# Kernel tuning notes

Hardware: AMD Instinct MI355X
Metric: run time of the kernel (lower is better)

Reference implementation:

```python
import jax, jax.numpy as jnp
import numpy as np

TOPK = 32
NUM_PT = 8192
NUM_KP = 8
HW = 19200


def _conv3(x, w, b):
    # x: [1, C, N], w: [O, C, 3] -> [1, O, N] (padding=1)
    y = jax.lax.conv_general_dilated(x, w, (1,), [(1, 1)],
                                     dimension_numbers=('NCH', 'OIH', 'NCH'))
    return y + b[None, :, None]


def setup_inputs() -> dict:
    key = jax.random.key(0)
    ks = jax.random.split(key, 64)

    def p(i, *shape):
        return (jax.random.normal(ks[i], shape, dtype=jnp.float32) * 0.05)

    inp = {
        'seg': jax.random.uniform(ks[0], (1, NUM_PT), dtype=jnp.float32),
        'img': jax.random.normal(ks[1], (1, 32, HW), dtype=jnp.float32),
        'cloud': jax.random.normal(ks[2], (1, NUM_PT, 3), dtype=jnp.float32),
        't': jax.random.normal(ks[3], (1, 3), dtype=jnp.float32),
        'choose': jax.random.randint(ks[4], (1, 1, NUM_PT), 0, HW),
        # Pseudo3DConv params (all 1x1 conv1d == channel matmul)
        'pconv1_w': p(5, 64, 3),    'pconv1_b': p(6, 64),
        'pconv2_w': p(7, 128, 64),  'pconv2_b': p(8, 128),
        'conv1_w': p(9, 64, 32),    'conv1_b': p(10, 64),
        'conv2_w': p(11, 128, 64),  'conv2_b': p(12, 128),
        'psconv1_w': p(13, 256, 128), 'psconv1_b': p(14, 256),
        'psconv2_w': p(15, 128, 256), 'psconv2_b': p(16, 128),
        'final_w': p(17, 128, 416), 'final_b': p(18, 128),
        # heads
        'seg1_w': p(19, 64, 128, 3), 'seg1_b': p(20, 64),
        'seg2_w': p(21, 32, 64),     'seg2_b': p(22, 32),
        'seg3_w': p(23, 1, 32),      'seg3_b': p(24, 1),
        'dis1_w': p(25, 64, 128, 3), 'dis1_b': p(26, 64),
        'dis2_w': p(27, 32, 64),     'dis2_b': p(28, 32),
        'dis3_w': p(29, 1, 32),      'dis3_b': p(30, 1),
        'lin1_w': p(31, 90, 128),    'lin1_b': p(32, 90),
        'lin2_w': p(33, 64, 90),     'lin2_b': p(34, 64),
        'lin3_w': p(35, 3 * NUM_KP, 64), 'lin3_b': p(36, 3 * NUM_KP),
    }
    return inp


def reference(seg, img, cloud, t, choose,
              pconv1_w, pconv1_b, pconv2_w, pconv2_b,
              conv1_w, conv1_b, conv2_w, conv2_b,
              psconv1_w, psconv1_b, psconv2_w, psconv2_b,
              final_w, final_b,
              seg1_w, seg1_b, seg2_w, seg2_b, seg3_w, seg3_b,
              dis1_w, dis1_b, dis2_w, dis2_b, dis3_w, dis3_b,
              lin1_w, lin1_b, lin2_w, lin2_b, lin3_w, lin3_b):
    lrelu = jax.nn.leaky_relu  # slope 0.01, same as torch default
    N = NUM_PT

    # gather per-point image features at chosen pixels: [N, 32]
    feat = jnp.take(img[0], choose[0, 0], axis=1).T
    c = cloud[0]  # [N, 3]

    # ---- KNN (self included, as in knn_cuda) ----
    d2 = jnp.sum((c[:, None, :] - c[None, :, :]) ** 2, axis=-1)  # [N, N]
    _, idx = jax.lax.top_k(-d2, TOPK)  # [N, K] nearest neighbors

    # ---- point-feature MLP (pconv1 -> lrelu -> pconv2) ----
    pf = lrelu(c @ pconv1_w.T + pconv1_b) @ pconv2_w.T + pconv2_b  # [N, 128]

    # ---- vectorized per-point neighbor gather + MLP + weighted maxpool ----
    nf = feat[idx]    # [N, K, 32]
    npf = pf[idx]     # [N, K, 128]
    npos = c[idx]     # [N, K, 3]
    w = jax.nn.softmax(-jnp.linalg.norm(c[:, None, :] - npos, axis=-1), axis=1)  # [N, K]

    f = lrelu(nf @ conv1_w.T + conv1_b) @ conv2_w.T + conv2_b          # [N, K, 128]
    fp = lrelu(npf @ psconv1_w.T + psconv1_b) @ psconv2_w.T + psconv2_b  # [N, K, 128]
    f = jnp.max(f * w[..., None], axis=1)    # [N, 128]
    fp = jnp.max(fp * w[..., None], axis=1)  # [N, 128]

    # final2 = [fp | img_feat], final1 = [f | cloud_feat] -> cat -> [N, 416]
    final = jnp.concatenate([fp, feat, f, pf], axis=1)
    fused = lrelu(final) @ final_w.T + final_b  # [N, 128]
    fused = fused.T[None]  # [1, 128, N]

    def pw(x, w_, b_):  # 1x1 conv1d on [1, C, N]
        return jnp.einsum('oc,bcn->bon', w_, x) + b_[None, :, None]

    # segmentation head
    h = lrelu(_conv3(fused, seg1_w, seg1_b))
    seg_pre = pw(lrelu(pw(h, seg2_w, seg2_b)), seg3_w, seg3_b).reshape(1, N)

    # distance-to-center weighting (norm along coord dim, softmax over points)
    dis_center = jax.nn.softmax(
        jnp.linalg.norm(cloud - (-t)[:, None, :], axis=2), axis=1)  # [1, N]

    # distance head (on unweighted fused features, matching torch op order)
    h = lrelu(_conv3(fused, dis1_w, dis1_b))
    dis_pre = pw(lrelu(pw(h, dis2_w, dis2_b)), dis3_w, dis3_b).reshape(1, N)

    # weight fused features by center distance and segmentation, sum-pool
    fused = fused * dis_center[:, None, :] * seg[:, None, :]
    g = jnp.sum(fused, axis=2)  # [1, 128]

    kp = lrelu(g @ lin1_w.T + lin1_b)
    kp = lrelu(kp @ lin2_w.T + lin2_b)
    keypoints = (kp @ lin3_w.T + lin3_b).reshape(1, NUM_KP, 3)
    return keypoints, dis_pre, dis_center, seg_pre
```

## Files before the change

kernel.cpp:

```cpp
#include <hip/hip_runtime.h>
#include <math.h>

#define NPT 8192
#define HWIMG 19200
#define KCAP 128

using short8 = __attribute__((ext_vector_type(8))) short;
using f32x4  = __attribute__((ext_vector_type(4))) float;

__device__ __forceinline__ float lrelu(float x) { return x > 0.f ? x : 0.01f * x; }
__device__ __forceinline__ unsigned short f2bf(float v) {
  unsigned u = __float_as_uint(v);
  return (unsigned short)((u + 0x7fffu + ((u >> 16) & 1u)) >> 16);
}
__device__ __forceinline__ float bf2f(unsigned short h) {
  return __uint_as_float(((unsigned)h) << 16);
}
__device__ __forceinline__ void split2(float v, unsigned short& h, unsigned short& l) {
  h = f2bf(v);
  l = f2bf(v - bf2f(h));
}
__device__ __forceinline__ void mfma3(f32x4& acc, short8 ah, short8 al, short8 wh, short8 wl) {
  acc = __builtin_amdgcn_mfma_f32_16x16x32_bf16(ah, wh, acc, 0, 0, 0);
  acc = __builtin_amdgcn_mfma_f32_16x16x32_bf16(al, wh, acc, 0, 0, 0);
  acc = __builtin_amdgcn_mfma_f32_16x16x32_bf16(ah, wl, acc, 0, 0, 0);
}

__device__ __forceinline__ int swz(int o, int k, int Kc) {
  return ((((o >> 4) * Kc + (k >> 5)) << 6) + (((k >> 3) & 3) << 4) + (o & 15)) * 8 + (k & 7);
}

#define OFF_PCONV2  0
#define OFF_CONV1   8192
#define OFF_CONV2   10240
#define OFF_PSCONV1 18432
#define OFF_PSCONV2 51200
#define OFF_FINAL   83968
#define OFF_W3      137216
#define OFF_W2P     186368

#define S_C4    NPT
#define S_G     129
#define S_BIASC 128
#define S_B2C   64
#define S_FEAT  (NPT*32)
#define S_W3    49152
#define S_W2P   8192
#define S_WSPL  OFF_W3
#define PREP_TOTAL (S_C4 + S_G + S_BIASC + S_B2C + S_FEAT + S_W3 + S_W2P + S_WSPL)
__global__ void k_prep(const float* __restrict__ cloud, const int* __restrict__ choose,
                       const float* __restrict__ img,
                       const float* __restrict__ seg1_w, const float* __restrict__ dis1_w,
                       const float* __restrict__ seg1_b, const float* __restrict__ dis1_b,
                       const float* __restrict__ seg2_w, const float* __restrict__ dis2_w,
                       const float* __restrict__ seg2_b, const float* __restrict__ dis2_b,
                       const float* __restrict__ pconv2_w, const float* __restrict__ conv1_w,
                       const float* __restrict__ conv2_w, const float* __restrict__ psconv1_w,
                       const float* __restrict__ psconv2_w, const float* __restrict__ final_w,
                       float* __restrict__ c4, float* __restrict__ g,
                       float* __restrict__ biasc, float* __restrict__ bias2c,
// ... 73 lines not shown

__device__ __forceinline__ unsigned bsort32u(unsigned key, int lane) {
#pragma unroll
  for (int k = 2; k <= 64; k <<= 1) {
#pragma unroll
    for (int j = k >> 1; j > 0; j >>= 1) {
      unsigned o = __shfl_xor(key, j, 64);
      bool keepmin = (((lane & j) == 0) == ((lane & k) == 0));
      key = ((o < key) == keepmin) ? o : key;
    }
  }
  return key;
}
__device__ __forceinline__ unsigned long long bsort64(unsigned long long key, int lane) {
#pragma unroll
  for (int k = 2; k <= 64; k <<= 1) {
#pragma unroll
    for (int j = k >> 1; j > 0; j >>= 1) {
      unsigned long long o = __shfl_xor(key, j, 64);
      bool keepmin = (((lane & j) == 0) == ((lane & k) == 0));
      bool omin = o < key;
      key = (omin == keepmin) ? o : key;
    }
  }
  return key;
}
__device__ __forceinline__ unsigned long long bmerge64(unsigned long long key, int lane) {
#pragma unroll
  for (int j = 32; j > 0; j >>= 1) {
    unsigned long long o = __shfl_xor(key, j, 64);
    bool keepmin = ((lane & j) == 0);
    bool omin = o < key;
    key = (omin == keepmin) ? o : key;
  }
  return key;
}

#define MEGA_GRID 3073
__global__ __launch_bounds__(256) void k_mega(const float4* __restrict__ c4,
                                              int* __restrict__ idxo, float* __restrict__ wo,
                                              const float* __restrict__ cloud,
                                              const float* __restrict__ tvec,
                                              float* __restrict__ dc,
                                              const float* __restrict__ pconv1_w, const float* __restrict__ pconv1_b,
                                              const float* __restrict__ pconv2_b, const float* __restrict__ psconv1_b,
                                              const float* __restrict__ psconv2_b,
                                              const unsigned short* __restrict__ feat_h,
                                              const unsigned short* __restrict__ feat_l,
                                              const float* __restrict__ conv1_b, const float* __restrict__ conv2_b,
                                              const unsigned short* __restrict__ Wh,
                                              const unsigned short* __restrict__ Wl,
                                              float* __restrict__ pf, float* __restrict__ Yfp,
                                              float* __restrict__ Yf) {
  __shared__ __align__(16) char smem[24704];
  int tid = threadIdx.x, lane = tid & 63, w = tid >> 6;
  int mr = lane & 15, q = lane >> 4;
  if (blockIdx.x > 2048) {
    unsigned short* sh_h = (unsigned short*)smem;
    unsigned short* sh_l = (unsigned short*)(smem + 12288);
    int cb = blockIdx.x - 2049;
    if (cb < 512) {
      int m0 = cb * 16;
      float4 cp = c4[m0 + mr];
      short8 ah0, al0, ah1, al1;
#pragma unroll
      for (int j = 0; j < 8; ++j) {
        int c0 = q*8 + j, c1 = 32 + q*8 + j;
        float v0 = lrelu(fmaf(cp.x, pconv1_w[c0*3+0], fmaf(cp.y, pconv1_w[c0*3+1],
                          fmaf(cp.z, pconv1_w[c0*3+2], pconv1_b[c0]))));
        float v1 = lrelu(fmaf(cp.x, pconv1_w[c1*3+0], fmaf(cp.y, pconv1_w[c1*3+1],
                          fmaf(cp.z, pconv1_w[c1*3+2], pconv1_b[c1]))));
        unsigned short hh, ll;
        split2(v0, hh, ll); ah0[j] = (short)hh; al0[j] = (short)ll;
        split2(v1, hh, ll); ah1[j] = (short)hh; al1[j] = (short)ll;
      }
      f32x4 acc[2];
#pragma unroll
      for (int t = 0; t < 2; ++t) { f32x4 z = {0.f,0.f,0.f,0.f}; acc[t] = z; }
      const unsigned short* W2h = Wh + OFF_PCONV2;
      const unsigned short* W2l = Wl + OFF_PCONV2;
#pragma unroll
      for (int tt = 0; tt < 2; ++tt) {
        int t1 = 2*w + tt;
        int w0 = ((t1*2 + 0)*64 + lane)*8, w1 = ((t1*2 + 1)*64 + lane)*8;
        mfma3(acc[tt], ah0, al0, *(const short8*)(W2h + w0), *(const short8*)(W2l + w0));
        mfma3(acc[tt], ah1, al1, *(const short8*)(W2h + w1), *(const short8*)(W2l + w1));
      }
#pragma unroll
      for (int tt = 0; tt < 2; ++tt) {
        int t1 = 2*w + tt, n = t1*16 + mr;
        float b = pconv2_b[n];
        int ks2 = t1 >> 1, q2 = (t1 & 1)*2 + (mr >> 3), jd = mr & 7;
#pragma unroll
        for (int r = 0; r < 4; ++r) {
          int row = q*4 + r;
          float v = acc[tt][r] + b;
          pf[(size_t)(m0+row)*128 + n] = v;
          unsigned short hh, ll; split2(v, hh, ll);
          int p = ((ks2*16 + row)*4 + q2)*8 + jd;
          sh_h[p] = hh; sh_l[p] = ll;
        }
      }
      __syncthreads();
      f32x4 acc2[4];
#pragma unroll
      for (int t = 0; t < 4; ++t) { f32x4 z = {0.f,0.f,0.f,0.f}; acc2[t] = z; }
      const unsigned short* W3h = Wh + OFF_PSCONV1;
      const unsigned short* W3l = Wl + OFF_PSCONV1;
#pragma unroll
      for (int ks = 0; ks < 4; ++ks) {
        int ap = ((ks*16 + mr)*4 + q)*8;
        short8 ah = *(const short8*)&sh_h[ap];
        short8 al = *(const short8*)&sh_l[ap];
#pragma unroll
        for (int tt = 0; tt < 4; ++tt) {
          int wb = (((4*w+tt)*4 + ks)*64 + lane)*8;
          mfma3(acc2[tt], ah, al, *(const short8*)(W3h + wb), *(const short8*)(W3l + wb));
        }
      }
      __syncthreads();
#pragma unroll
      for (int tt = 0; tt < 4; ++tt) {
        int t2 = 4*w + tt, n = t2*16 + mr;
        float b = psconv1_b[n];
        int ks3 = t2 >> 1, q3 = (t2 & 1)*2 + (mr >> 3), jd = mr & 7;
#pragma unroll
        for (int r = 0; r < 4; ++r) {
          int row = q*4 + r;
          float v = lrelu(acc2[tt][r] + b);
          unsigned short hh, ll; split2(v, hh, ll);
          int p = 6144 + ((ks3*16 + row)*4 + q3)*8 + jd;
          sh_h[p] = hh; sh_l[p] = ll;
        }
      }
      __syncthreads();
      f32x4 acc3[2];
#pragma unroll
      for (int t = 0; t < 2; ++t) { f32x4 z = {0.f,0.f,0.f,0.f}; acc3[t] = z; }
      const unsigned short* W4h = Wh + OFF_PSCONV2;
      const unsigned short* W4l = Wl + OFF_PSCONV2;
#pragma unroll
      for (int ks = 0; ks < 8; ++ks) {
        int ap = 6144 + ((ks*16 + mr)*4 + q)*8;
        short8 ah = *(const short8*)&sh_h[ap];
        short8 al = *(const short8*)&sh_l[ap];
#pragma unroll
        for (int tt = 0; tt < 2; ++tt) {
          int wb = (((2*w+tt)*8 + ks)*64 + lane)*8;
          mfma3(acc3[tt], ah, al, *(const short8*)(W4h + wb), *(const short8*)(W4l + wb));
        }
      }
#pragma unroll
      for (int tt = 0; tt < 2; ++tt) {
        int n = (2*w+tt)*16 + mr;
        float b = psconv2_b[n];
#pragma unroll
        for (int r = 0; r < 4; ++r)
          Yfp[(size_t)(m0 + q*4 + r)*128 + n] = acc3[tt][r] + b;
      }
    } else {
      int m0 = (cb - 512) * 16;
      int ab = ((m0 >> 4)*64 + lane)*8;
      short8 ah = *(const short8*)(feat_h + ab);
      short8 al = *(const short8*)(feat_l + ab);
      f32x4 acc = {0.f,0.f,0.f,0.f};
      const unsigned short* W1h = Wh + OFF_CONV1;
      const unsigned short* W1l = Wl + OFF_CONV1;
      {
        int wb = (w*64 + lane)*8;
        mfma3(acc, ah, al, *(const short8*)(W1h + wb), *(const short8*)(W1l + wb));
      }
      {
        int n = w*16 + mr;
        float b = conv1_b[n];
        int ks2 = n >> 5, q2 = (n >> 3) & 3, jd = mr & 7;
#pragma unroll
        for (int r = 0; r < 4; ++r) {
          int row = q*4 + r;
          float v = lrelu(acc[r] + b);
          unsigned short hh, ll; split2(v, hh, ll);
          int p = ((ks2*16 + row)*4 + q2)*8 + jd;
          sh_h[p] = hh; sh_l[p] = ll;
        }
      }
      __syncthreads();
      f32x4 acc2[2];
#pragma unroll
      for (int t = 0; t < 2; ++t) { f32x4 z = {0.f,0.f,0.f,0.f}; acc2[t] = z; }
      const unsigned short* W2h = Wh + OFF_CONV2;
      const unsigned short* W2l = Wl + OFF_CONV2;
#pragma unroll
      for (int ks = 0; ks < 2; ++ks) {
        int ap = ((ks*16 + mr)*4 + q)*8;
        short8 a2 = *(const short8*)&sh_h[ap];
        short8 a2l = *(const short8*)&sh_l[ap];
#pragma unroll
        for (int tt = 0; tt < 2; ++tt) {
          int wb = (((2*w+tt)*2 + ks)*64 + lane)*8;
          mfma3(acc2[tt], a2, a2l, *(const short8*)(W2h + wb), *(const short8*)(W2l + wb));
        }
      }
#pragma unroll
      for (int tt = 0; tt < 2; ++tt) {
// ... 63 lines not shown
    float4 vv = *(const float4*)&smin[w][lane*4];
    float m4 = fmaxf(fminf(fminf(vv.x, vv.y), fminf(vv.z, vv.w)), 0.f);
    unsigned key = bsort32u(__float_as_uint(m4), lane);
    float T = __uint_as_float(__shfl(key, 31, 64));
    if (lane == 0) sTv[w] = T * (1.f + 2e-5f) + 4e-5f;
  }
  __syncthreads();
  float T0 = sTv[0], T1 = sTv[1], T2 = sTv[2], T3 = sTv[3];
  for (int t = 0; t < 32; ++t) {
    int j = t*256 + tid;
    float4 cj = c4[j];
    float d;
#define APPEND(Q, P) { \
    float dx_ = (P).x-cj.x, dy_ = (P).y-cj.y, dz_ = (P).z-cj.z; \
    float de_ = dx_*dx_ + dy_*dy_ + dz_*dz_; \
    int p_ = atomicAdd(&scnt[Q],1); if (p_ < KCAP) { sd[Q][p_] = de_; sj[Q][p_] = j; } }
    d = DDOT(p0x,p0y,p0z,p0.w,cj); if (d <= T0) APPEND(0, p0);
    d = DDOT(p1x,p1y,p1z,p1.w,cj); if (d <= T1) APPEND(1, p1);
    d = DDOT(p2x,p2y,p2z,p2.w,cj); if (d <= T2) APPEND(2, p2);
    d = DDOT(p3x,p3y,p3z,p3.w,cj); if (d <= T3) APPEND(3, p3);
  }
  __syncthreads();
  int M = scnt[w]; if (M > KCAP) M = KCAP;
  unsigned long long key = (lane < M)
      ? (((unsigned long long)__float_as_uint(sd[w][lane]) << 32) | (unsigned)sj[w][lane])
      : ~0ull;
  key = bsort64(key, lane);
  for (int base = 64; base < M; base += 64) {
    unsigned long long nk = (base + lane < M)
        ? (((unsigned long long)__float_as_uint(sd[w][base+lane]) << 32) | (unsigned)sj[w][base+lane])
        : ~0ull;
    nk = bsort64(nk, lane);
    nk = __shfl_xor(nk, 63, 64);
    key = key < nk ? key : nk;
    key = bmerge64(key, lane);
  }
  float dsel = __uint_as_float((unsigned)(key >> 32));
  int   jsel = (int)(unsigned)(key & 0xffffffffu);
  float v = -sqrtf(dsel);
  float mx = v;
#pragma unroll
  for (int o = 1; o < 32; o <<= 1) mx = fmaxf(mx, __shfl_xor(mx, o, 64));
  float e = expf(v - mx);
  float s = e;
#pragma unroll
  for (int o = 1; o < 32; o <<= 1) s += __shfl_xor(s, o, 64);
  if (lane < 32) {
    int qd = q0 + w;
    wo[qd*32 + lane] = e / s;
    idxo[qd*32 + lane] = jsel;
  }
}

__global__ __launch_bounds__(256) void k_pool(const float* __restrict__ Yf,
                                              const float* __restrict__ Yfp,
                                              const float* __restrict__ feat,
                                              const float* __restrict__ pf,
                                              const int* __restrict__ idx,
                                              const float* __restrict__ w,
                                              unsigned short* __restrict__ finh,
                                              unsigned short* __restrict__ finl) {
  int n = blockIdx.x;
  int tid = threadIdx.x;
  __shared__ int sj[32];
  __shared__ float sw[32];
  __shared__ float part[2][4][128];
  __shared__ float sfin[416];
  if (tid < 32) { sj[tid] = idx[n*32+tid]; sw[tid] = w[n*32+tid]; }
  __syncthreads();
  int arr = tid >> 7, kq = (tid >> 5) & 3, cg = tid & 31;
  const float* Y = arr ? Yf : Yfp;
  float4 acc = {-INFINITY, -INFINITY, -INFINITY, -INFINITY};
#pragma unroll
  for (int kk = 0; kk < 8; ++kk) {
    int k = kq*8 + kk;
    float4 v = *(const float4*)&Y[(size_t)sj[k]*128 + cg*4];
    float wk = sw[k];
    acc.x = fmaxf(acc.x, wk*v.x); acc.y = fmaxf(acc.y, wk*v.y);
    acc.z = fmaxf(acc.z, wk*v.z); acc.w = fmaxf(acc.w, wk*v.w);
  }
  *(float4*)&part[arr][kq][cg*4] = acc;
  __syncthreads();
  if (tid < 64) {
    int a2 = tid >> 5, c2 = tid & 31;
    float4 m0v = *(const float4*)&part[a2][0][c2*4];
    float4 m1v = *(const float4*)&part[a2][1][c2*4];
    float4 m2v = *(const float4*)&part[a2][2][c2*4];
    float4 m3v = *(const float4*)&part[a2][3][c2*4];
    int base = a2 ? 160 : 0;
    sfin[base + c2*4 + 0] = lrelu(fmaxf(fmaxf(m0v.x, m1v.x), fmaxf(m2v.x, m3v.x)));
    sfin[base + c2*4 + 1] = lrelu(fmaxf(fmaxf(m0v.y, m1v.y), fmaxf(m2v.y, m3v.y)));
    sfin[base + c2*4 + 2] = lrelu(fmaxf(fmaxf(m0v.z, m1v.z), fmaxf(m2v.z, m3v.z)));
    sfin[base + c2*4 + 3] = lrelu(fmaxf(fmaxf(m0v.w, m1v.w), fmaxf(m2v.w, m3v.w)));
  } else if (tid < 192) {
    int c = tid - 64;
    sfin[288 + c] = lrelu(pf[n*128 + c]);
  } else if (tid < 224) {
    int c = tid - 192;
    sfin[128 + c] = lrelu(feat[n*32 + c]);
  }
  __syncthreads();
  if (tid < 104) {
    int plane = tid >= 52;
    int ck = plane ? tid - 52 : tid;
    int ks = ck >> 2, qq = ck & 3;
    int c0 = ks*32 + qq*8;
    short8 o8;
#pragma unroll
    for (int j = 0; j < 8; ++j) {
      unsigned short hh, ll; split2(sfin[c0 + j], hh, ll);
      o8[j] = (short)(plane ? ll : hh);
    }
    size_t pos = (((size_t)(n >> 4)*13 + ks)*64 + qq*16 + (n & 15))*8;
    *(short8*)((plane ? finl : finh) + pos) = o8;
  }
}

__global__ __launch_bounds__(256) void k_final(const unsigned short* __restrict__ Ah,
                                              const unsigned short* __restrict__ Al,
                                              const unsigned short* __restrict__ Wh,
                                              const unsigned short* __restrict__ Wl,
                                              const float* __restrict__ bias,
                                              unsigned short* __restrict__ Ch,
                                              unsigned short* __restrict__ Cl) {
  __shared__ float sC[16][132];
  int tid = threadIdx.x, lane = tid & 63, w = tid >> 6;
  int mr = lane & 15, q = lane >> 4;
  int mt = blockIdx.x;
  f32x4 acc[2];
#pragma unroll
  for (int t = 0; t < 2; ++t) { f32x4 z = {0.f,0.f,0.f,0.f}; acc[t] = z; }
#pragma unroll
  for (int ks = 0; ks < 13; ++ks) {
    int ab = ((mt*13 + ks)*64 + lane)*8;
    short8 ah = *(const short8*)(Ah + ab);
    short8 al = *(const short8*)(Al + ab);
#pragma unroll
    for (int tt = 0; tt < 2; ++tt) {
      int wb = (((2*w+tt)*13 + ks)*64 + lane)*8;
      mfma3(acc[tt], ah, al, *(const short8*)(Wh + wb), *(const short8*)(Wl + wb));
    }
  }
#pragma unroll
  for (int tt = 0; tt < 2; ++tt) {
    int n = (2*w+tt)*16 + mr;
    float b = bias[n];
#pragma unroll
    for (int r = 0; r < 4; ++r) sC[q*4 + r][n] = acc[tt][r] + b;
  }
  __syncthreads();
  {
    int ks = tid >> 6, q2 = (tid >> 4) & 3, mr2 = tid & 15;
    int c0 = ks*32 + q2*8;
    short8 oh, ol;
#pragma unroll
    for (int j = 0; j < 8; ++j) {
      unsigned short hh, ll; split2(sC[mr2][c0 + j], hh, ll);
      oh[j] = (short)hh; ol[j] = (short)ll;
    }
    size_t pos = ((size_t)mt*256 + tid)*8;
    *(short8*)(Ch + pos) = oh;
    *(short8*)(Cl + pos) = ol;
  }
}

__global__ __launch_bounds__(256) void k_c3head(const unsigned short* __restrict__ Ah,
                                               const unsigned short* __restrict__ Al,
                                               const unsigned short* __restrict__ Wh,
                                               const unsigned short* __restrict__ Wl,
                                               const float* __restrict__ biasc,
                                               const float* __restrict__ bias2c,
                                               const float* __restrict__ segw, const float* __restrict__ segb,
                                               const float* __restrict__ disw, const float* __restrict__ disb,
                                               float* __restrict__ osegp, float* __restrict__ odisp,
                                               const float* __restrict__ dc,
                                               const float* __restrict__ seg,
                                               float* __restrict__ g,
                                               const float* __restrict__ l1w, const float* __restrict__ l1b,
                                               const float* __restrict__ l2w, const float* __restrict__ l2b,
                                               const float* __restrict__ l3w, const float* __restrict__ l3b,
                                               float* __restrict__ o_kp) {
  int tid = threadIdx.x, lane = tid & 63, w = tid >> 6;
  int mr = lane & 15, q = lane >> 4;
  if (blockIdx.x >= 512) {
    __shared__ float sred[2048];
    __shared__ int slast;
    int b = blockIdx.x - 512;
    float pg[8] = {0.f,0.f,0.f,0.f,0.f,0.f,0.f,0.f};
    int mrr = tid & 15;
    for (int mi = 0; mi < 16; ++mi) {
      int m = b*16 + mi;
      int row = m*16 + mrr;
      float wrow = dc[row] * seg[row];
      size_t pos = ((size_t)m*256 + tid)*8;
      short8 hv = *(const short8*)(Ah + pos);
      short8 lv = *(const short8*)(Al + pos);
#pragma unroll
      for (int j = 0; j < 8; ++j)
        pg[j] += (bf2f((unsigned short)hv[j]) + bf2f((unsigned short)lv[j])) * wrow;
    }
#pragma unroll
    for (int j = 0; j < 8; ++j) sred[tid*8 + j] = pg[j];
    __syncthreads();
    if (tid < 128) {
      int ks = tid >> 5, q2 = (tid >> 3) & 3, j = tid & 7;
      float s = 0.f;
#pragma unroll
      for (int mr2 = 0; mr2 < 16; ++mr2) s += sred[((ks<<6) + (q2<<4) + mr2)*8 + j];
      atomicAdd(&g[tid], s);
    }
    __threadfence();
    __syncthreads();
    if (tid == 0) slast = (atomicAdd((int*)(g + 128), 1) == 31);
    __syncthreads();
    if (!slast) return;
    __shared__ float sg[128], s1[90], s2[64];
    if (tid < 128) sg[tid] = atomicAdd(&g[tid], 0.f);
    __syncthreads();
    if (tid < 90) {
      float a = l1b[tid];
      for (int i = 0; i < 128; ++i) a += sg[i]*l1w[tid*128+i];
      s1[tid] = lrelu(a);
    }
    __syncthreads();
    if (tid < 64) {
      float a = l2b[tid];
      for (int i = 0; i < 90; ++i) a += s1[i]*l2w[tid*90+i];
      s2[tid] = lrelu(a);
    }
    __syncthreads();
    if (tid < 24) {
      float a = l3b[tid];
      for (int i = 0; i < 64; ++i) a += s2[i]*l3w[tid*64+i];
      o_kp[tid] = a;
    }
    return;
  }
  __shared__ unsigned short t1h[2048], t1l[2048];
  __shared__ float shead[4][16][17];
  int m0 = blockIdx.x * 16;
  f32x4 acc[2];
#pragma unroll
  for (int t = 0; t < 2; ++t) { f32x4 z = {0.f,0.f,0.f,0.f}; acc[t] = z; }
  const unsigned short* W3h = Wh + OFF_W3;
  const unsigned short* W3l = Wl + OFF_W3;
#pragma unroll
  for (int ks = 0; ks < 12; ++ks) {
    int tap = ks >> 2, ksA = ks & 3;
    int ar = m0 + mr + tap - 1;
    short8 ah = {0,0,0,0,0,0,0,0}, al = {0,0,0,0,0,0,0,0};
    if (ar >= 0 && ar < NPT) {
      int ab = ((((ar >> 4)*4) + ksA)*64 + q*16 + (ar & 15))*8;
      ah = *(const short8*)(Ah + ab);
      al = *(const short8*)(Al + ab);
    }
#pragma unroll
    for (int tt = 0; tt < 2; ++tt) {
      int wb = (((2*w+tt)*12 + ks)*64 + lane)*8;
      mfma3(acc[tt], ah, al, *(const short8*)(W3h + wb), *(const short8*)(W3l + wb));
    }
  }
#pragma unroll
  for (int tt = 0; tt < 2; ++tt) {
    int t2 = 2*w + tt, n = t2*16 + mr;
    float b = biasc[n];
    int ks2 = t2 >> 1, q2 = (t2 & 1)*2 + (mr >> 3), jd = mr & 7;
#pragma unroll
    for (int r = 0; r < 4; ++r) {
      int row = q*4 + r;
      float v = lrelu(acc[tt][r] + b);
      unsigned short hh, ll; split2(v, hh, ll);
      int p = ((ks2*16 + row)*4 + q2)*8 + jd;
      t1h[p] = hh; t1l[p] = ll;
    }
  }
  __syncthreads();
  f32x4 acc2 = {0.f,0.f,0.f,0.f};
  const unsigned short* WPh = Wh + OFF_W2P;
  const unsigned short* WPl = Wl + OFF_W2P;
#pragma unroll
  for (int ks = 0; ks < 4; ++ks) {
    int ap = ((ks*16 + mr)*4 + q)*8;
    short8 ah = *(const short8*)&t1h[ap];
    short8 al = *(const short8*)&t1l[ap];
    int wb = ((w*4 + ks)*64 + lane)*8;
    mfma3(acc2, ah, al, *(const short8*)(WPh + wb), *(const short8*)(WPl + wb));
  }
  float hw = (w < 2) ? segw[w*16 + mr] : disw[(w-2)*16 + mr];
  float bb = bias2c[w*16 + mr];
#pragma unroll
  for (int r = 0; r < 4; ++r)
    shead[w][q*4 + r][mr] = lrelu(acc2[r] + bb) * hw;
  __syncthreads();
  if (tid < 16) {
    float a = 0.f;
#pragma unroll
    for (int i = 0; i < 16; ++i) a += shead[0][tid][i] + shead[1][tid][i];
    osegp[m0 + tid] = a + segb[0];
  } else if (tid < 32) {
    float a = 0.f;
#pragma unroll
    for (int i = 0; i < 16; ++i) a += shead[2][tid-16][i] + shead[3][tid-16][i];
    odisp[m0 + tid - 16] = a + disb[0];
  }
}

extern "C" void kernel_launch(void* const* d_in, const int* in_sizes, int n_in,
                              void* d_out, int out_size, void* d_ws, size_t ws_size,
                              hipStream_t stream) {
  const float* seg      = (const float*)d_in[0];
  const float* img      = (const float*)d_in[1];
  const float* cloud    = (const float*)d_in[2];
  const float* tvec     = (const float*)d_in[3];
  const int*   choose   = (const int*)d_in[4];
  const float* pconv1_w = (const float*)d_in[5];
  const float* pconv1_b = (const float*)d_in[6];
  const float* pconv2_w = (const float*)d_in[7];
  const float* pconv2_b = (const float*)d_in[8];
  const float* conv1_w  = (const float*)d_in[9];
  const float* conv1_b  = (const float*)d_in[10];
  const float* conv2_w  = (const float*)d_in[11];
  const float* conv2_b  = (const float*)d_in[12];
  const float* psconv1_w= (const float*)d_in[13];
  const float* psconv1_b= (const float*)d_in[14];
  const float* psconv2_w= (const float*)d_in[15];
  const float* psconv2_b= (const float*)d_in[16];
  const float* final_w  = (const float*)d_in[17];
  const float* final_b  = (const float*)d_in[18];
  const float* seg1_w   = (const float*)d_in[19];
  const float* seg1_b   = (const float*)d_in[20];
  const float* seg2_w   = (const float*)d_in[21];
  const float* seg2_b   = (const float*)d_in[22];
  const float* seg3_w   = (const float*)d_in[23];
  const float* seg3_b   = (const float*)d_in[24];
  const float* dis1_w   = (const float*)d_in[25];
  const float* dis1_b   = (const float*)d_in[26];
  const float* dis2_w   = (const float*)d_in[27];
  const float* dis2_b   = (const float*)d_in[28];
  const float* dis3_w   = (const float*)d_in[29];
  const float* dis3_b   = (const float*)d_in[30];
  const float* lin1_w   = (const float*)d_in[31];
  const float* lin1_b   = (const float*)d_in[32];
  const float* lin2_w   = (const float*)d_in[33];
  const float* lin2_b   = (const float*)d_in[34];
  const float* lin3_w   = (const float*)d_in[35];
  const float* lin3_b   = (const float*)d_in[36];

  float* out = (float*)d_out;
  float* ws  = (float*)d_ws;

  float* c4     = ws + 0;
  float* feat   = ws + 32768;
  unsigned short* feat_h = (unsigned short*)(ws + 294912);
  unsigned short* feat_l = (unsigned short*)(ws + 425984);
  float* pf     = ws + 557056;
  float* Yf     = ws + 1605632;
  float* Yfp    = ws + 2654208;
  int*   idx    = (int*)(ws + 3702784);
  float* wsm    = ws + 3964928;
  unsigned short* finh  = (unsigned short*)(ws + 4227072);
  unsigned short* finl  = (unsigned short*)(ws + 5931008);
  unsigned short* fusedh = (unsigned short*)(ws + 8683520);
  unsigned short* fusedl = (unsigned short*)(ws + 9207808);
  unsigned short* Wh    = (unsigned short*)(ws + 9732096);
  unsigned short* Wl    = (unsigned short*)(ws + 9829376);
  float* biasc  = ws + 9926656;
  float* bias2c = ws + 9926784;
  float* g      = ws + 9926848;

  float* o_kp   = out;
  float* o_disp = out + 24;
  float* o_dc   = out + 8216;
  float* o_segp = out + 16408;

  k_prep<<<(PREP_TOTAL + 255)/256, 256, 0, stream>>>(
      cloud, choose, img, seg1_w, dis1_w, seg1_b, dis1_b,
      seg2_w, dis2_w, seg2_b, dis2_b,
      pconv2_w, conv1_w, conv2_w, psconv1_w, psconv2_w, final_w,
      c4, g, biasc, bias2c, feat, feat_h, feat_l, Wh, Wl);

  k_mega<<<MEGA_GRID, 256, 0, stream>>>(
      (const float4*)c4, idx, wsm, cloud, tvec, o_dc,
      pconv1_w, pconv1_b, pconv2_b, psconv1_b, psconv2_b,
      feat_h, feat_l, conv1_b, conv2_b, Wh, Wl, pf, Yfp, Yf);

  k_pool<<<NPT, 256, 0, stream>>>(Yf, Yfp, feat, pf, idx, wsm, finh, finl);

  k_final<<<512, 256, 0, stream>>>(finh, finl, Wh + OFF_FINAL, Wl + OFF_FINAL,
                                   final_b, fusedh, fusedl);

  k_c3head<<<544, 256, 0, stream>>>(fusedh, fusedl, Wh, Wl, biasc, bias2c,
                                    seg3_w, seg3_b, dis3_w, dis3_b, o_segp, o_disp,
                                    o_dc, seg, g,
                                    lin1_w, lin1_b, lin2_w, lin2_b, lin3_w, lin3_b, o_kp);

  (void)in_sizes; (void)n_in; (void)out_size; (void)ws_size;
}
```

Before: 238.5 us.

## Fuse pooling, final projection and conv3 heads into one tiled tail kernel

Replaces the separate pool, final-projection and conv3-head kernels with one kernel per 16-point tile. It recomputes the max-pool and final projection for a one-point halo on each side so the 3-tap conv can read neighbours from shared memory, and it drops the finh/finl round trip through global memory. The global-feature reduction moves into its own small kernel. Separately, the psconv1→psconv2 chain in the mega kernel is split into two halves to shrink shared memory, which may raise occupancy. The cost is redundant halo work (18 rows per 16), fewer blocks in the tail (512 instead of 8192 pool blocks), and an extra sync per half.

```diff
diff --git a/kernel.cpp b/kernel.cpp
--- a/kernel.cpp
+++ b/kernel.cpp
@@ -6,6 +6,7 @@
 #define KCAP 128
 
 using short8 = __attribute__((ext_vector_type(8))) short;
+using short4v = __attribute__((ext_vector_type(4))) short;
 using f32x4  = __attribute__((ext_vector_type(4))) float;
 
 __device__ __forceinline__ float lrelu(float x) { return x > 0.f ? x : 0.01f * x; }
@@ -185,12 +186,12 @@
                                               const unsigned short* __restrict__ Wl,
                                               float* __restrict__ pf, float* __restrict__ Yfp,
                                               float* __restrict__ Yf) {
-  __shared__ __align__(16) char smem[24704];
+  __shared__ __align__(16) char smem[16384];
   int tid = threadIdx.x, lane = tid & 63, w = tid >> 6;
   int mr = lane & 15, q = lane >> 4;
   if (blockIdx.x > 2048) {
     unsigned short* sh_h = (unsigned short*)smem;
-    unsigned short* sh_l = (unsigned short*)(smem + 12288);
+    unsigned short* sh_l = (unsigned short*)(smem + 8192);
     int cb = blockIdx.x - 2049;
     if (cb < 512) {
       int m0 = cb * 16;
@@ -235,53 +236,58 @@
         }
       }
       __syncthreads();
-      f32x4 acc2[4];
-#pragma unroll
-      for (int t = 0; t < 4; ++t) { f32x4 z = {0.f,0.f,0.f,0.f}; acc2[t] = z; }
+      f32x4 acc3[2];
+#pragma unroll
+      for (int t = 0; t < 2; ++t) { f32x4 z = {0.f,0.f,0.f,0.f}; acc3[t] = z; }
       const unsigned short* W3h = Wh + OFF_PSCONV1;
       const unsigned short* W3l = Wl + OFF_PSCONV1;
-#pragma unroll
-      for (int ks = 0; ks < 4; ++ks) {
-        int ap = ((ks*16 + mr)*4 + q)*8;
-        short8 ah = *(const short8*)&sh_h[ap];
-        short8 al = *(const short8*)&sh_l[ap];
-#pragma unroll
-        for (int tt = 0; tt < 4; ++tt) {
-          int wb = (((4*w+tt)*4 + ks)*64 + lane)*8;
-          mfma3(acc2[tt], ah, al, *(const short8*)(W3h + wb), *(const short8*)(W3l + wb));
-        }
-      }
-      __syncthreads();
-#pragma unroll
-      for (int tt = 0; tt < 4; ++tt) {
-        int t2 = 4*w + tt, n = t2*16 + mr;
-        float b = psconv1_b[n];
-        int ks3 = t2 >> 1, q3 = (t2 & 1)*2 + (mr >> 3), jd = mr & 7;
-#pragma unroll
-        for (int r = 0; r < 4; ++r) {
-          int row = q*4 + r;
-          float v = lrelu(acc2[tt][r] + b);
-          unsigned short hh, ll; split2(v, hh, ll);
-          int p = 6144 + ((ks3*16 + row)*4 + q3)*8 + jd;
-          sh_h[p] = hh; sh_l[p] = ll;
-        }
-      }
-      __syncthreads();
-      f32x4 acc3[2];
-#pragma unroll
-      for (int t = 0; t < 2; ++t) { f32x4 z = {0.f,0.f,0.f,0.f}; acc3[t] = z; }
       const unsigned short* W4h = Wh + OFF_PSCONV2;
       const unsigned short* W4l = Wl + OFF_PSCONV2;
 #pragma unroll
-      for (int ks = 0; ks < 8; ++ks) {
-        int ap = 6144 + ((ks*16 + mr)*4 + q)*8;
-        short8 ah = *(const short8*)&sh_h[ap];
-        short8 al = *(const short8*)&sh_l[ap];
+      for (int h = 0; h < 2; ++h) {
+        f32x4 acc2[2];
+#pragma unroll
+        for (int t = 0; t < 2; ++t) { f32x4 z = {0.f,0.f,0.f,0.f}; acc2[t] = z; }
+#pragma unroll
+        for (int ks = 0; ks < 4; ++ks) {
+          int ap = ((ks*16 + mr)*4 + q)*8;
+          short8 ah = *(const short8*)&sh_h[ap];
+          short8 al = *(const short8*)&sh_l[ap];
+#pragma unroll
+          for (int tt = 0; tt < 2; ++tt) {
+            int ts = h*8 + 2*w + tt;
+            int wb = ((ts*4 + ks)*64 + lane)*8;
+            mfma3(acc2[tt], ah, al, *(const short8*)(W3h + wb), *(const short8*)(W3l + wb));
+          }
+        }
 #pragma unroll
         for (int tt = 0; tt < 2; ++tt) {
-          int wb = (((2*w+tt)*8 + ks)*64 + lane)*8;
-          mfma3(acc3[tt], ah, al, *(const short8*)(W4h + wb), *(const short8*)(W4l + wb));
+          int tl = 2*w + tt;
+          int n = h*128 + tl*16 + mr;
+          float b = psconv1_b[n];
+          int ks3 = tl >> 1, q3 = (tl & 1)*2 + (mr >> 3), jd = mr & 7;
+#pragma unroll
+          for (int r = 0; r < 4; ++r) {
+            int row = q*4 + r;
+            float v = lrelu(acc2[tt][r] + b);
+            unsigned short hh, ll; split2(v, hh, ll);
+            int p = 2048 + ((ks3*16 + row)*4 + q3)*8 + jd;
+            sh_h[p] = hh; sh_l[p] = ll;
+          }
         }
+        __syncthreads();
+#pragma unroll
+        for (int ks = 0; ks < 4; ++ks) {
+          int ap = 2048 + ((ks*16 + mr)*4 + q)*8;
+          short8 ah = *(const short8*)&sh_h[ap];
+          short8 al = *(const short8*)&sh_l[ap];
+#pragma unroll
+          for (int tt = 0; tt < 2; ++tt) {
+            int wb = (((2*w+tt)*8 + h*4 + ks)*64 + lane)*8;
+            mfma3(acc3[tt], ah, al, *(const short8*)(W4h + wb), *(const short8*)(W4l + wb));
+          }
+        }
+        __syncthreads();
       }
 #pragma unroll
       for (int tt = 0; tt < 2; ++tt) {
@@ -451,212 +457,153 @@
   }
 }
 
-__global__ __launch_bounds__(256) void k_pool(const float* __restrict__ Yf,
+__global__ __launch_bounds__(256) void k_tail(const float* __restrict__ Yf,
                                               const float* __restrict__ Yfp,
                                               const float* __restrict__ feat,
                                               const float* __restrict__ pf,
                                               const int* __restrict__ idx,
-                                              const float* __restrict__ w,
-                                              unsigned short* __restrict__ finh,
-                                              unsigned short* __restrict__ finl) {
-  int n = blockIdx.x;
-  int tid = threadIdx.x;
-  __shared__ int sj[32];
-  __shared__ float sw[32];
-  __shared__ float part[2][4][128];
-  __shared__ float sfin[416];
-  if (tid < 32) { sj[tid] = idx[n*32+tid]; sw[tid] = w[n*32+tid]; }
-  __syncthreads();
-  int arr = tid >> 7, kq = (tid >> 5) & 3, cg = tid & 31;
-  const float* Y = arr ? Yf : Yfp;
-  float4 acc = {-INFINITY, -INFINITY, -INFINITY, -INFINITY};
-#pragma unroll
-  for (int kk = 0; kk < 8; ++kk) {
-    int k = kq*8 + kk;
-    float4 v = *(const float4*)&Y[(size_t)sj[k]*128 + cg*4];
-    float wk = sw[k];
-    acc.x = fmaxf(acc.x, wk*v.x); acc.y = fmaxf(acc.y, wk*v.y);
-    acc.z = fmaxf(acc.z, wk*v.z); acc.w = fmaxf(acc.w, wk*v.w);
-  }
-  *(float4*)&part[arr][kq][cg*4] = acc;
-  __syncthreads();
-  if (tid < 64) {
-    int a2 = tid >> 5, c2 = tid & 31;
-    float4 m0v = *(const float4*)&part[a2][0][c2*4];
-    float4 m1v = *(const float4*)&part[a2][1][c2*4];
-    float4 m2v = *(const float4*)&part[a2][2][c2*4];
-    float4 m3v = *(const float4*)&part[a2][3][c2*4];
-    int base = a2 ? 160 : 0;
-    sfin[base + c2*4 + 0] = lrelu(fmaxf(fmaxf(m0v.x, m1v.x), fmaxf(m2v.x, m3v.x)));
-    sfin[base + c2*4 + 1] = lrelu(fmaxf(fmaxf(m0v.y, m1v.y), fmaxf(m2v.y, m3v.y)));
-    sfin[base + c2*4 + 2] = lrelu(fmaxf(fmaxf(m0v.z, m1v.z), fmaxf(m2v.z, m3v.z)));
-    sfin[base + c2*4 + 3] = lrelu(fmaxf(fmaxf(m0v.w, m1v.w), fmaxf(m2v.w, m3v.w)));
-  } else if (tid < 192) {
-    int c = tid - 64;
-    sfin[288 + c] = lrelu(pf[n*128 + c]);
-  } else if (tid < 224) {
-    int c = tid - 192;
-    sfin[128 + c] = lrelu(feat[n*32 + c]);
-  }
-  __syncthreads();
-  if (tid < 104) {
-    int plane = tid >= 52;
-    int ck = plane ? tid - 52 : tid;
-    int ks = ck >> 2, qq = ck & 3;
-    int c0 = ks*32 + qq*8;
-    short8 o8;
-#pragma unroll
-    for (int j = 0; j < 8; ++j) {
-      unsigned short hh, ll; split2(sfin[c0 + j], hh, ll);
-      o8[j] = (short)(plane ? ll : hh);
-    }
-    size_t pos = (((size_t)(n >> 4)*13 + ks)*64 + qq*16 + (n & 15))*8;
-    *(short8*)((plane ? finl : finh) + pos) = o8;
-  }
-}
-
-__global__ __launch_bounds__(256) void k_final(const unsigned short* __restrict__ Ah,
-                                              const unsigned short* __restrict__ Al,
+                                              const float* __restrict__ wsm,
                                               const unsigned short* __restrict__ Wh,
                                               const unsigned short* __restrict__ Wl,
-                                              const float* __restrict__ bias,
-                                              unsigned short* __restrict__ Ch,
-                                              unsigned short* __restrict__ Cl) {
-  __shared__ float sC[16][132];
+                                              const float* __restrict__ final_b,
+                                              const float* __restrict__ biasc,
+                                              const float* __restrict__ bias2c,
+                                              const float* __restrict__ segw, const float* __restrict__ segb,
+                                              const float* __restrict__ disw, const float* __restrict__ disb,
+                                              unsigned short* __restrict__ fusedh,
+                                              unsigned short* __restrict__ fusedl,
+                                              float* __restrict__ osegp, float* __restrict__ odisp) {
+  __shared__ int sjn[18][32];
+  __shared__ float swn[18][32];
+  __shared__ __align__(16) char sbuf[37440];
   int tid = threadIdx.x, lane = tid & 63, w = tid >> 6;
   int mr = lane & 15, q = lane >> 4;
-  int mt = blockIdx.x;
-  f32x4 acc[2];
-#pragma unroll
-  for (int t = 0; t < 2; ++t) { f32x4 z = {0.f,0.f,0.f,0.f}; acc[t] = z; }
+  int mt = blockIdx.x, m0 = mt * 16;
+  for (int t = tid; t < 18*32; t += 256) {
+    int lr = t >> 5, k = t & 31, gr = m0 - 1 + lr;
+    if (gr >= 0 && gr < NPT) { sjn[lr][k] = idx[gr*32+k]; swn[lr][k] = wsm[gr*32+k]; }
+    else { sjn[lr][k] = 0; swn[lr][k] = 0.f; }
+  }
+  __syncthreads();
+  for (int t = tid; t < 1872; t += 256) {
+    int lr, col;
+    float4 v4;
+    if (t < 1152) {
+      lr = t >> 6; int arr = (t >> 5) & 1, cg = t & 31;
+      const float* Y = arr ? Yf : Yfp;
+      float ax = -INFINITY, ay = -INFINITY, az = -INFINITY, aw = -INFINITY;
+#pragma unroll 8
+      for (int k = 0; k < 32; ++k) {
+        float4 vv = *(const float4*)&Y[(size_t)sjn[lr][k]*128 + cg*4];
+        float wk = swn[lr][k];
+        ax = fmaxf(ax, wk*vv.x); ay = fmaxf(ay, wk*vv.y);
+        az = fmaxf(az, wk*vv.z); aw = fmaxf(aw, wk*vv.w);
+      }
+      v4.x = lrelu(ax); v4.y = lrelu(ay); v4.z = lrelu(az); v4.w = lrelu(aw);
+      col = (arr ? 160 : 0) + cg*4;
+    } else if (t < 1728) {
+      int u = t - 1152; lr = u >> 5; int cg = u & 31;
+      int gr = m0 - 1 + lr;
+      int gc = gr < 0 ? 0 : (gr >= NPT ? NPT-1 : gr);
+      float4 p4 = *(const float4*)&pf[(size_t)gc*128 + cg*4];
+      v4.x = lrelu(p4.x); v4.y = lrelu(p4.y); v4.z = lrelu(p4.z); v4.w = lrelu(p4.w);
+      col = 288 + cg*4;
+    } else {
+      int u = t - 1728; lr = u >> 3; int cg = u & 7;
+      int gr = m0 - 1 + lr;
+      int gc = gr < 0 ? 0 : (gr >= NPT ? NPT-1 : gr);
+      float4 p4 = *(const float4*)&feat[(size_t)gc*32 + cg*4];
+      v4.x = lrelu(p4.x); v4.y = lrelu(p4.y); v4.z = lrelu(p4.z); v4.w = lrelu(p4.w);
+      col = 128 + cg*4;
+    }
+    int gr = m0 - 1 + lr;
+    if (gr < 0 || gr >= NPT) { v4.x = 0.f; v4.y = 0.f; v4.z = 0.f; v4.w = 0.f; }
+    int ks = col >> 5, qq = (col >> 3) & 3, j0 = col & 7;
+    char* base = sbuf + (ks*18 + lr)*80 + qq*16 + j0*2;
+    short4v hv, lv;
+    unsigned short hh, ll;
+    split2(v4.x, hh, ll); hv[0] = (short)hh; lv[0] = (short)ll;
+    split2(v4.y, hh, ll); hv[1] = (short)hh; lv[1] = (short)ll;
+    split2(v4.z, hh, ll); hv[2] = (short)hh; lv[2] = (short)ll;
+    split2(v4.w, hh, ll); hv[3] = (short)hh; lv[3] = (short)ll;
+    *(short4v*)base = hv;
+    *(short4v*)(base + 18720) = lv;
+  }
+  __syncthreads();
+  f32x4 accA[2], accB[2];
+#pragma unroll
+  for (int t = 0; t < 2; ++t) {
+    f32x4 z = {0.f,0.f,0.f,0.f}; accA[t] = z; accB[t] = z;
+  }
+  const unsigned short* WFh = Wh + OFF_FINAL;
+  const unsigned short* WFl = Wl + OFF_FINAL;
 #pragma unroll
   for (int ks = 0; ks < 13; ++ks) {
-    int ab = ((mt*13 + ks)*64 + lane)*8;
-    short8 ah = *(const short8*)(Ah + ab);
-    short8 al = *(const short8*)(Al + ab);
+    int arB = 16 + mr; if (arB > 17) arB = 17;
+    const char* pA = sbuf + (ks*18 + mr)*80 + q*16;
+    const char* pB = sbuf + (ks*18 + arB)*80 + q*16;
+    short8 ahA = *(const short8*)pA;
+    short8 alA = *(const short8*)(pA + 18720);
+    short8 ahB = *(const short8*)pB;
+    short8 alB = *(const short8*)(pB + 18720);
 #pragma unroll
     for (int tt = 0; tt < 2; ++tt) {
       int wb = (((2*w+tt)*13 + ks)*64 + lane)*8;
-      mfma3(acc[tt], ah, al, *(const short8*)(Wh + wb), *(const short8*)(Wl + wb));
-    }
-  }
-#pragma unroll
-  for (int tt = 0; tt < 2; ++tt) {
-    int n = (2*w+tt)*16 + mr;
-    float b = bias[n];
-#pragma unroll
-    for (int r = 0; r < 4; ++r) sC[q*4 + r][n] = acc[tt][r] + b;
+      short8 wh = *(const short8*)(WFh + wb);
+      short8 wl = *(const short8*)(WFl + wb);
+      mfma3(accA[tt], ahA, alA, wh, wl);
+      mfma3(accB[tt], ahB, alB, wh, wl);
+    }
+  }
+  __syncthreads();
+#pragma unroll
+  for (int tile = 0; tile < 2; ++tile) {
+#pragma unroll
+    for (int tt = 0; tt < 2; ++tt) {
+      int t2 = 2*w + tt, n = t2*16 + mr;
+      float b = final_b[n];
+      int ksA = t2 >> 1, qq = (t2 & 1)*2 + (mr >> 3), jd = mr & 7;
+#pragma unroll
+      for (int r = 0; r < 4; ++r) {
+        int lr = tile*16 + q*4 + r;
+        if (lr > 17) continue;
+        int gr = m0 - 1 + lr;
+        float v = (tile ? accB[tt][r] : accA[tt][r]) + b;
+        if (gr < 0 || gr >= NPT) v = 0.f;
+        unsigned short hh, ll; split2(v, hh, ll);
+        char* p = sbuf + (ksA*18 + lr)*80 + qq*16 + jd*2;
+        *(unsigned short*)p = hh;
+        *(unsigned short*)(p + 5760) = ll;
+      }
+    }
   }
   __syncthreads();
   {
-    int ks = tid >> 6, q2 = (tid >> 4) & 3, mr2 = tid & 15;
-    int c0 = ks*32 + q2*8;
-    short8 oh, ol;
-#pragma unroll
-    for (int j = 0; j < 8; ++j) {
-      unsigned short hh, ll; split2(sC[mr2][c0 + j], hh, ll);
-      oh[j] = (short)hh; ol[j] = (short)ll;
-    }
+    int ks2 = tid >> 6, q2 = (tid >> 4) & 3, mr2 = tid & 15;
+    int lr = mr2 + 1;
+    const char* p = sbuf + (ks2*18 + lr)*80 + q2*16;
+    short8 oh = *(const short8*)p;
+    short8 ol = *(const short8*)(p + 5760);
     size_t pos = ((size_t)mt*256 + tid)*8;
-    *(short8*)(Ch + pos) = oh;
-    *(short8*)(Cl + pos) = ol;
-  }
-}
-
-__global__ __launch_bounds__(256) void k_c3head(const unsigned short* __restrict__ Ah,
-                                               const unsigned short* __restrict__ Al,
-                                               const unsigned short* __restrict__ Wh,
-                                               const unsigned short* __restrict__ Wl,
-                                               const float* __restrict__ biasc,
-                                               const float* __restrict__ bias2c,
-                                               const float* __restrict__ segw, const float* __restrict__ segb,
-                                               const float* __restrict__ disw, const float* __restrict__ disb,
-                                               float* __restrict__ osegp, float* __restrict__ odisp,
-                                               const float* __restrict__ dc,
-                                               const float* __restrict__ seg,
-                                               float* __restrict__ g,
-                                               const float* __restrict__ l1w, const float* __restrict__ l1b,
-                                               const float* __restrict__ l2w, const float* __restrict__ l2b,
-                                               const float* __restrict__ l3w, const float* __restrict__ l3b,
-                                               float* __restrict__ o_kp) {
-  int tid = threadIdx.x, lane = tid & 63, w = tid >> 6;
-  int mr = lane & 15, q = lane >> 4;
-  if (blockIdx.x >= 512) {
-    __shared__ float sred[2048];
-    __shared__ int slast;
-    int b = blockIdx.x - 512;
-    float pg[8] = {0.f,0.f,0.f,0.f,0.f,0.f,0.f,0.f};
-    int mrr = tid & 15;
-    for (int mi = 0; mi < 16; ++mi) {
-      int m = b*16 + mi;
-      int row = m*16 + mrr;
-      float wrow = dc[row] * seg[row];
-      size_t pos = ((size_t)m*256 + tid)*8;
-      short8 hv = *(const short8*)(Ah + pos);
-      short8 lv = *(const short8*)(Al + pos);
-#pragma unroll
-      for (int j = 0; j < 8; ++j)
-        pg[j] += (bf2f((unsigned short)hv[j]) + bf2f((unsigned short)lv[j])) * wrow;
-    }
-#pragma unroll
-    for (int j = 0; j < 8; ++j) sred[tid*8 + j] = pg[j];
-    __syncthreads();
-    if (tid < 128) {
-      int ks = tid >> 5, q2 = (tid >> 3) & 3, j = tid & 7;
-      float s = 0.f;
-#pragma unroll
-      for (int mr2 = 0; mr2 < 16; ++mr2) s += sred[((ks<<6) + (q2<<4) + mr2)*8 + j];
-      atomicAdd(&g[tid], s);
-    }
-    __threadfence();
-    __syncthreads();
-    if (tid == 0) slast = (atomicAdd((int*)(g + 128), 1) == 31);
-    __syncthreads();
-    if (!slast) return;
-    __shared__ float sg[128], s1[90], s2[64];
-    if (tid < 128) sg[tid] = atomicAdd(&g[tid], 0.f);
-    __syncthreads();
-    if (tid < 90) {
-      float a = l1b[tid];
-      for (int i = 0; i < 128; ++i) a += sg[i]*l1w[tid*128+i];
-      s1[tid] = lrelu(a);
-    }
-    __syncthreads();
-    if (tid < 64) {
-      float a = l2b[tid];
-      for (int i = 0; i < 90; ++i) a += s1[i]*l2w[tid*90+i];
-      s2[tid] = lrelu(a);
-    }
-    __syncthreads();
-    if (tid < 24) {
-      float a = l3b[tid];
-      for (int i = 0; i < 64; ++i) a += s2[i]*l3w[tid*64+i];
-      o_kp[tid] = a;
-    }
-    return;
-  }
-  __shared__ unsigned short t1h[2048], t1l[2048];
-  __shared__ float shead[4][16][17];
-  int m0 = blockIdx.x * 16;
-  f32x4 acc[2];
-#pragma unroll
-  for (int t = 0; t < 2; ++t) { f32x4 z = {0.f,0.f,0.f,0.f}; acc[t] = z; }
+    *(short8*)(fusedh + pos) = oh;
+    *(short8*)(fusedl + pos) = ol;
+  }
+  f32x4 acc3[2];
+#pragma unroll
+  for (int t = 0; t < 2; ++t) { f32x4 z = {0.f,0.f,0.f,0.f}; acc3[t] = z; }
   const unsigned short* W3h = Wh + OFF_W3;
   const unsigned short* W3l = Wl + OFF_W3;
 #pragma unroll
   for (int ks = 0; ks < 12; ++ks) {
     int tap = ks >> 2, ksA = ks & 3;
-    int ar = m0 + mr + tap - 1;
-    short8 ah = {0,0,0,0,0,0,0,0}, al = {0,0,0,0,0,0,0,0};
-    if (ar >= 0 && ar < NPT) {
-      int ab = ((((ar >> 4)*4) + ksA)*64 + q*16 + (ar & 15))*8;
-      ah = *(const short8*)(Ah + ab);
-      al = *(const short8*)(Al + ab);
-    }
+    int ar = mr + tap;
+    const char* p = sbuf + (ksA*18 + ar)*80 + q*16;
+    short8 ah = *(const short8*)p;
+    short8 al = *(const short8*)(p + 5760);
 #pragma unroll
     for (int tt = 0; tt < 2; ++tt) {
       int wb = (((2*w+tt)*12 + ks)*64 + lane)*8;
-      mfma3(acc[tt], ah, al, *(const short8*)(W3h + wb), *(const short8*)(W3l + wb));
+      mfma3(acc3[tt], ah, al, *(const short8*)(W3h + wb), *(const short8*)(W3l + wb));
     }
   }
 #pragma unroll
@@ -667,40 +614,106 @@
 #pragma unroll
     for (int r = 0; r < 4; ++r) {
       int row = q*4 + r;
-      float v = lrelu(acc[tt][r] + b);
+      float v = lrelu(acc3[tt][r] + b);
       unsigned short hh, ll; split2(v, hh, ll);
-      int p = ((ks2*16 + row)*4 + q2)*8 + jd;
-      t1h[p] = hh; t1l[p] = ll;
-    }
-  }
-  __syncthreads();
-  f32x4 acc2 = {0.f,0.f,0.f,0.f};
+      char* p = sbuf + 11520 + (ks2*16 + row)*80 + q2*16 + jd*2;
+      *(unsigned short*)p = hh;
+      *(unsigned short*)(p + 5120) = ll;
+    }
+  }
+  __syncthreads();
+  f32x4 acc4 = {0.f,0.f,0.f,0.f};
   const unsigned short* WPh = Wh + OFF_W2P;
   const unsigned short* WPl = Wl + OFF_W2P;
 #pragma unroll
   for (int ks = 0; ks < 4; ++ks) {
-    int ap = ((ks*16 + mr)*4 + q)*8;
-    short8 ah = *(const short8*)&t1h[ap];
-    short8 al = *(const short8*)&t1l[ap];
+    const char* p = sbuf + 11520 + (ks*16 + mr)*80 + q*16;
+    short8 ah = *(const short8*)p;
+    short8 al = *(const short8*)(p + 5120);
     int wb = ((w*4 + ks)*64 + lane)*8;
-    mfma3(acc2, ah, al, *(const short8*)(WPh + wb), *(const short8*)(WPl + wb));
+    mfma3(acc4, ah, al, *(const short8*)(WPh + wb), *(const short8*)(WPl + wb));
   }
   float hw = (w < 2) ? segw[w*16 + mr] : disw[(w-2)*16 + mr];
   float bb = bias2c[w*16 + mr];
+  float* shead = (float*)(sbuf + 21760);
 #pragma unroll
   for (int r = 0; r < 4; ++r)
-    shead[w][q*4 + r][mr] = lrelu(acc2[r] + bb) * hw;
+    shead[(w*16 + q*4 + r)*17 + mr] = lrelu(acc4[r] + bb) * hw;
   __syncthreads();
   if (tid < 16) {
     float a = 0.f;
 #pragma unroll
-    for (int i = 0; i < 16; ++i) a += shead[0][tid][i] + shead[1][tid][i];
+    for (int i = 0; i < 16; ++i) a += shead[(tid)*17 + i] + shead[(16 + tid)*17 + i];
     osegp[m0 + tid] = a + segb[0];
   } else if (tid < 32) {
+    int r2 = tid - 16;
     float a = 0.f;
 #pragma unroll
-    for (int i = 0; i < 16; ++i) a += shead[2][tid-16][i] + shead[3][tid-16][i];
-    odisp[m0 + tid - 16] = a + disb[0];
+    for (int i = 0; i < 16; ++i) a += shead[(32 + r2)*17 + i] + shead[(48 + r2)*17 + i];
+    odisp[m0 + r2] = a + disb[0];
+  }
+}
+
+__global__ __launch_bounds__(256) void k_gk(const unsigned short* __restrict__ Ah,
+                                            const unsigned short* __restrict__ Al,
+                                            const float* __restrict__ dc,
+                                            const float* __restrict__ seg,
+                                            float* __restrict__ g,
+                                            const float* __restrict__ l1w, const float* __restrict__ l1b,
+                                            const float* __restrict__ l2w, const float* __restrict__ l2b,
+                                            const float* __restrict__ l3w, const float* __restrict__ l3b,
+                                            float* __restrict__ o_kp) {
+  __shared__ float sred[2048];
+  __shared__ int slast;
+  int tid = threadIdx.x;
+  int b = blockIdx.x;
+  float pg[8] = {0.f,0.f,0.f,0.f,0.f,0.f,0.f,0.f};
+  int mrr = tid & 15;
+  for (int mi = 0; mi < 16; ++mi) {
+    int m = b*16 + mi;
+    int row = m*16 + mrr;
+    float wrow = dc[row] * seg[row];
+    size_t pos = ((size_t)m*256 + tid)*8;
+    short8 hv = *(const short8*)(Ah + pos);
+    short8 lv = *(const short8*)(Al + pos);
+#pragma unroll
+    for (int j = 0; j < 8; ++j)
+      pg[j] += (bf2f((unsigned short)hv[j]) + bf2f((unsigned short)lv[j])) * wrow;
+  }
+#pragma unroll
+  for (int j = 0; j < 8; ++j) sred[tid*8 + j] = pg[j];
+  __syncthreads();
+  if (tid < 128) {
+    int ks = tid >> 5, q2 = (tid >> 3) & 3, j = tid & 7;
+    float s = 0.f;
+#pragma unroll
+    for (int mr2 = 0; mr2 < 16; ++mr2) s += sred[((ks<<6) + (q2<<4) + mr2)*8 + j];
+    atomicAdd(&g[tid], s);
+  }
+  __threadfence();
+  __syncthreads();
+  if (tid == 0) slast = (atomicAdd((int*)(g + 128), 1) == 31);
+  __syncthreads();
+  if (!slast) return;
+  __shared__ float sg[128], s1[90], s2[64];
+  if (tid < 128) sg[tid] = atomicAdd(&g[tid], 0.f);
+  __syncthreads();
+  if (tid < 90) {
+    float a = l1b[tid];
+    for (int i = 0; i < 128; ++i) a += sg[i]*l1w[tid*128+i];
+    s1[tid] = lrelu(a);
+  }
+  __syncthreads();
+  if (tid < 64) {
+    float a = l2b[tid];
+    for (int i = 0; i < 90; ++i) a += s1[i]*l2w[tid*90+i];
+    s2[tid] = lrelu(a);
+  }
+  __syncthreads();
+  if (tid < 24) {
+    float a = l3b[tid];
+    for (int i = 0; i < 64; ++i) a += s2[i]*l3w[tid*64+i];
+    o_kp[tid] = a;
   }
 }
 
@@ -757,8 +770,6 @@
   float* Yfp    = ws + 2654208;
   int*   idx    = (int*)(ws + 3702784);
   float* wsm    = ws + 3964928;
-  unsigned short* finh  = (unsigned short*)(ws + 4227072);
-  unsigned short* finl  = (unsigned short*)(ws + 5931008);
   unsigned short* fusedh = (unsigned short*)(ws + 8683520);
   unsigned short* fusedl = (unsigned short*)(ws + 9207808);
   unsigned short* Wh    = (unsigned short*)(ws + 9732096);
@@ -783,15 +794,13 @@
       pconv1_w, pconv1_b, pconv2_b, psconv1_b, psconv2_b,
       feat_h, feat_l, conv1_b, conv2_b, Wh, Wl, pf, Yfp, Yf);
 
-  k_pool<<<NPT, 256, 0, stream>>>(Yf, Yfp, feat, pf, idx, wsm, finh, finl);
-
-  k_final<<<512, 256, 0, stream>>>(finh, finl, Wh + OFF_FINAL, Wl + OFF_FINAL,
-                                   final_b, fusedh, fusedl);
-
-  k_c3head<<<544, 256, 0, stream>>>(fusedh, fusedl, Wh, Wl, biasc, bias2c,
-                                    seg3_w, seg3_b, dis3_w, dis3_b, o_segp, o_disp,
-                                    o_dc, seg, g,
-                                    lin1_w, lin1_b, lin2_w, lin2_b, lin3_w, lin3_b, o_kp);
+  k_tail<<<512, 256, 0, stream>>>(
+      Yf, Yfp, feat, pf, idx, wsm, Wh, Wl,
+      final_b, biasc, bias2c, seg3_w, seg3_b, dis3_w, dis3_b,
+      fusedh, fusedl, o_segp, o_disp);
+
+  k_gk<<<32, 256, 0, stream>>>(fusedh, fusedl, o_dc, seg, g,
+                               lin1_w, lin1_b, lin2_w, lin2_b, lin3_w, lin3_b, o_kp);
 
   (void)in_sizes; (void)n_in; (void)out_size; (void)ws_size;
 }
```

New measurement: 230.0 us. -3.6%, faster.
